# Optimization experiments

Measured on AMD Instinct MI355X. Metric: run time of the kernel, lower is better.

Reference implementation:

```python
import jax, jax.numpy as jnp
import numpy as np

EPS = 1e-3  # BatchNorm eps from partial(nn.BatchNorm1d, eps=0.001)


def _bn(x, g, b, m, v):
    # inference-mode BatchNorm1d with running stats
    return (x - m) * jax.lax.rsqrt(v + EPS) * g + b


def setup_inputs() -> dict:
    key = jax.random.key(0)
    ks = jax.random.split(key, 24)
    N_REF, N_Q, E = 50_000, 50_000, 1_600_000
    C_IN, C0, C1 = 16, 32, 32
    s = 0.1
    return {
        "ref_bxyz": jax.random.normal(ks[0], (N_REF, 4), jnp.float32),
        "ref_feat": jax.random.normal(ks[1], (N_REF, C_IN), jnp.float32),
        "query_bxyz": jax.random.normal(ks[2], (N_Q, 4), jnp.float32),
        "e_ref": jax.random.randint(ks[3], (E,), 0, N_REF, jnp.int32),
        "e_query": jax.random.randint(ks[4], (E,), 0, N_Q, jnp.int32),
        "w_pos": jax.random.normal(ks[5], (3, C0), jnp.float32) * s,
        "bn0_g": jax.random.uniform(ks[6], (C0,), jnp.float32, 0.5, 1.5),
        "bn0_b": jax.random.normal(ks[7], (C0,), jnp.float32) * s,
        "bn0_m": jax.random.normal(ks[8], (C0,), jnp.float32) * s,
        "bn0_v": jax.random.uniform(ks[9], (C0,), jnp.float32, 0.5, 1.5),
        "w_feat": jax.random.normal(ks[10], (C_IN, C0), jnp.float32) * s,
        "bnf_g": jax.random.uniform(ks[11], (C0,), jnp.float32, 0.5, 1.5),
        "bnf_b": jax.random.normal(ks[12], (C0,), jnp.float32) * s,
        "bnf_m": jax.random.normal(ks[13], (C0,), jnp.float32) * s,
        "bnf_v": jax.random.uniform(ks[14], (C0,), jnp.float32, 0.5, 1.5),
        "w1": jax.random.normal(ks[15], (C0, C1), jnp.float32) * s,
        "b1": jax.random.normal(ks[16], (C1,), jnp.float32) * s,
        "bn1_g": jax.random.uniform(ks[17], (C1,), jnp.float32, 0.5, 1.5),
        "bn1_b": jax.random.normal(ks[18], (C1,), jnp.float32) * s,
        "bn1_m": jax.random.normal(ks[19], (C1,), jnp.float32) * s,
        "bn1_v": jax.random.uniform(ks[20], (C1,), jnp.float32, 0.5, 1.5),
    }


def reference(ref_bxyz, ref_feat, query_bxyz, e_ref, e_query,
              w_pos, bn0_g, bn0_b, bn0_m, bn0_v,
              w_feat, bnf_g, bnf_b, bnf_m, bnf_v,
              w1, b1, bn1_g, bn1_b, bn1_m, bn1_v):
    # gather: per-edge xyz difference (drop batch column 0)
    pos_diff = (ref_bxyz[e_ref] - query_bxyz[e_query])[:, 1:4]        # [E, 3]
    pos_feat = _bn(pos_diff @ w_pos, bn0_g, bn0_b, bn0_m, bn0_v)       # [E, C0]
    # node-level feature projection, then gather per edge
    ref_feat2 = _bn(ref_feat @ w_feat, bnf_g, bnf_b, bnf_m, bnf_v)     # [N_ref, C0]
    edge_feat = jax.nn.relu(pos_feat + ref_feat2[e_ref])               # [E, C0]
    # mlp_convs chain (single layer here: C0 -> C1 with bias)
    edge_feat = jax.nn.relu(_bn(edge_feat @ w1 + b1, bn1_g, bn1_b, bn1_m, bn1_v))  # [E, C1]
    # scatter-max aggregate into query nodes; empty segments -> 0 (torch_scatter semantics)
    n_q = query_bxyz.shape[0]
    q = jax.ops.segment_max(edge_feat, e_query, num_segments=n_q)      # [N_q, C1]
    return jnp.where(jnp.isfinite(q), q, jnp.zeros((), q.dtype))
```

## Files before the change

### kernel.cpp

```cpp
#include <hip/hip_runtime.h>

#define EPS 1e-3f
#define FRAG_OFF 1184
#define PK_OFF 1696
#define NSUP 32
#define SUPSLOTS 69632
#define BINB 1024
#define WCAP 48
#define WRITERS 32
#define FCAP 1536
#define NFINE 2048

using frag_ab = __attribute__((ext_vector_type(8))) short;
using frag_cd = __attribute__((ext_vector_type(4))) float;
using iv4     = __attribute__((ext_vector_type(4))) int;

__device__ __forceinline__ unsigned pack_bf16_rne(float a, float b) {
    unsigned ua = __float_as_uint(a), ub = __float_as_uint(b);
    ua += 0x7FFFu + ((ua >> 16) & 1u);
    ub += 0x7FFFu + ((ub >> 16) & 1u);
    return (ua >> 16) | (ub & 0xFFFF0000u);
}
__device__ __forceinline__ unsigned cvt_pk_bf16(float a, float b) {
    unsigned r;
    asm("v_cvt_pk_bf16_f32 %0, %1, %2" : "=v"(r) : "v"(a), "v"(b));
    return r;
}
__device__ __forceinline__ float ubf_lo(unsigned u) { return __uint_as_float(u << 16); }
__device__ __forceinline__ float ubf_hi(unsigned u) { return __uint_as_float(u & 0xFFFF0000u); }

__global__ __launch_bounds__(256)
void mega_pre(const float* __restrict__ w_pos,
              const float* __restrict__ g0, const float* __restrict__ b0,
              const float* __restrict__ m0, const float* __restrict__ v0,
              const float* __restrict__ w1, const float* __restrict__ b1lin,
              const float* __restrict__ g1, const float* __restrict__ b1bn,
              const float* __restrict__ m1, const float* __restrict__ v1,
              const float* __restrict__ feat, const float* __restrict__ wf,
              const float* __restrict__ gf, const float* __restrict__ bf,
              const float* __restrict__ mf, const float* __restrict__ vf,
              const float4* __restrict__ bxyz,
              const int* __restrict__ e_query, const int* __restrict__ e_ref,
              float* __restrict__ ws, unsigned* __restrict__ ref2pk,
              uint2* __restrict__ pos_pk, int* __restrict__ supCur,
              unsigned* __restrict__ fineCnt, unsigned* __restrict__ pairs1,
              int E, int n_ref, int nodeB, int posB) {
    __shared__ unsigned bkt[4 * NSUP * WCAP];
    __shared__ int cnt[4 * NSUP];
    __shared__ int gb[NSUP], woff[4 * NSUP];

    int b = blockIdx.x, t = threadIdx.x;

    if (b == 0) {
        for (int i = t; i < NFINE; i += 256) fineCnt[i] = 0;
        if (t < 32) {
            int c = t;
            float s0 = g0[c] * rsqrtf(v0[c] + EPS);
            #pragma unroll
            for (int k = 0; k < 3; ++k) ws[k * 32 + c] = w_pos[k * 32 + c] * s0;
            ws[96 + c] = b0[c] - m0[c] * s0;
            float s1 = g1[c] * rsqrtf(v1[c] + EPS);
            #pragma unroll
            for (int k = 0; k < 32; ++k) ws[128 + k * 32 + c] = w1[k * 32 + c] * s1;
            ws[1152 + c] = (b1lin[c] - m1[c]) * s1 + b1bn[c];
        }
        __syncthreads();
        if (t < 64) {
            unsigned* wB = (unsigned*)ws + FRAG_OFF;
            int n = t & 15, quad = t >> 4;
            #pragma unroll
            for (int h = 0; h < 2; ++h) {
                int col = n + 16 * h;
                #pragma unroll
                for (int jp = 0; jp < 4; ++jp) {
                    int k = quad * 8 + 2 * jp;
                    wB[h * 256 + t * 4 + jp] =
                        pack_bf16_rne(ws[128 + k * 32 + col], ws[128 + (k + 1) * 32 + col]);
                }
            }
        }
        return;
    }
    b -= 1;
    if (b < nodeB) {
        int idx = b * 256 + t;
        if (idx < n_ref * 16) {
            int n = idx >> 4, cp = idx & 15;
            float fr[16];
            const float4* f4 = (const float4*)(feat + (size_t)n * 16);
            *(float4*)(fr)      = f4[0];
            *(float4*)(fr + 4)  = f4[1];
            *(float4*)(fr + 8)  = f4[2];
            *(float4*)(fr + 12) = f4[3];
            const float2* wf2 = (const float2*)wf;
            float a0 = 0.f, a1 = 0.f;
            #pragma unroll
            for (int k = 0; k < 16; ++k) {
                float2 wk = wf2[k * 16 + cp];
                a0 = fmaf(fr[k], wk.x, a0);
                a1 = fmaf(fr[k], wk.y, a1);
            }
            int c0 = 2 * cp, c1 = 2 * cp + 1;
            float s0 = gf[c0] * rsqrtf(vf[c0] + EPS);
            float s1 = gf[c1] * rsqrtf(vf[c1] + EPS);
            ref2pk[idx] = pack_bf16_rne((a0 - mf[c0]) * s0 + bf[c0],
                                        (a1 - mf[c1]) * s1 + bf[c1]);
        }
        return;
    }
    b -= nodeB;
    if (b < posB) {
        int i = b * 256 + t;
        if (i < n_ref) {
            float4 rb = bxyz[i];
            pos_pk[i] = make_uint2(pack_bf16_rne(rb.y, rb.z), pack_bf16_rne(rb.w, 0.f));
        }
        return;
    }
    b -= posB;
    int wv = t >> 6, lane = t & 63;
    if (t < 4 * NSUP) cnt[t] = 0;
    __syncthreads();
    int per = (((E + BINB * 4 - 1) / (BINB * 4)) + 3) & ~3;
    int gid = b * 4 + wv;
    int e0 = gid * per, e1 = min(e0 + per, E);
    for (int e = e0 + lane * 4; e < e1; e += 256) {
        if (e + 4 <= e1) {
            iv4 q4 = __builtin_nontemporal_load((const iv4*)(e_query + e));
            iv4 r4 = __builtin_nontemporal_load((const iv4*)(e_ref + e));
            #pragma unroll
            for (int j = 0; j < 4; ++j) {
                int q = q4[j], r = r4[j];
                int s = q >> 11;
                int pos = atomicAdd(&cnt[wv * NSUP + s], 1);
                if (pos < WCAP) bkt[wv * (NSUP * WCAP) + s * WCAP + pos] =
                    ((unsigned)(q & 2047) << 16) | (unsigned)r;
            }
        } else {
            for (int j = e; j < e1; ++j) {
                int q = e_query[j], r = e_ref[j];
                int s = q >> 11;
                int pos = atomicAdd(&cnt[wv * NSUP + s], 1);
                if (pos < WCAP) bkt[wv * (NSUP * WCAP) + s * WCAP + pos] =
                    ((unsigned)(q & 2047) << 16) | (unsigned)r;
            }
        }
    }
    __syncthreads();
    if (t < NSUP) {
        int s = t;
        int n0 = min(cnt[s], WCAP),            n1 = min(cnt[NSUP + s], WCAP);
        int n2 = min(cnt[2 * NSUP + s], WCAP), n3 = min(cnt[3 * NSUP + s], WCAP);
        woff[s] = 0; woff[NSUP + s] = n0;
        woff[2 * NSUP + s] = n0 + n1; woff[3 * NSUP + s] = n0 + n1 + n2;
        gb[s] = (n0 + n1 + n2 + n3) ? atomicAdd(&supCur[s], n0 + n1 + n2 + n3) : 0;
    }
    __syncthreads();
    for (int s = 0; s < NSUP; ++s) {
        int n = min(cnt[wv * NSUP + s], WCAP);
        if (lane < n) {
            int g = gb[s] + woff[wv * NSUP + s] + lane;
            if (g < SUPSLOTS)
                pairs1[(size_t)s * SUPSLOTS + g] = bkt[wv * (NSUP * WCAP) + s * WCAP + lane];
        }
    }
}

__global__ __launch_bounds__(256)
void finesort(const int* __restrict__ supCur, const unsigned* __restrict__ pairs1,
              unsigned* __restrict__ fineCnt, unsigned* __restrict__ pairs2) {
    __shared__ int h[64];
    __shared__ unsigned cb[64];
    __shared__ int lcnt[64];
    int s = blockIdx.x / WRITERS, w = blockIdx.x % WRITERS, t = threadIdx.x;
    if (t < 64) { h[t] = 0; lcnt[t] = 0; }
    __syncthreads();
    int n = min(supCur[s], SUPSLOTS);
    int lo = (n * w) / WRITERS, hi = (n * (w + 1)) / WRITERS;
    const unsigned* base = pairs1 + (size_t)s * SUPSLOTS;
    for (int i = lo + t; i < hi; i += 256)
        atomicAdd(&h[(base[i] >> 21) & 63], 1);
    __syncthreads();
    if (t < 64 && h[t] > 0)
        cb[t] = atomicAdd(&fineCnt[s * 64 + t], (unsigned)h[t]);
    __syncthreads();
    for (int i = lo + t; i < hi; i += 256) {
        unsigned u = base[i];
        int f = (u >> 21) & 63;
        unsigned pos = cb[f] + (unsigned)atomicAdd(&lcnt[f], 1);
        if (pos < FCAP)
            pairs2[(size_t)(s * 64 + f) * FCAP + pos] = u & 0x001FFFFFu;
    }
}

__global__ __launch_bounds__(512)
void fused_kernel(const uint2* __restrict__ pos_pk, const float4* __restrict__ query_bxyz,
                  const unsigned* __restrict__ fineCnt, const unsigned* __restrict__ pairs2,
                  const float* __restrict__ ws, float* __restrict__ out, int n_q) {
    __shared__ int outacc[32 * 33];
    __shared__ float4 qx[32];

    int t = threadIdx.x;
    int ln = t & 63, wv = t >> 6;
    int b = blockIdx.x;
    int q0 = b * 32;

    unsigned nc = fineCnt[b];
    int w = (int)(nc < FCAP ? nc : FCAP);
    const unsigned* __restrict__ src = pairs2 + (size_t)b * FCAP;
    if (t < 32) {
        int qq = q0 + t;
        qx[t] = query_bxyz[qq < n_q ? qq : 0];
    }
    for (int i = t; i < 32 * 33; i += 512) outacc[i] = 0;

    int mrow = ln & 15, cpg = ln >> 4;
    const float4* wsf4 = (const float4*)ws;
    float4 w0xa = wsf4[cpg * 2],          w0xb = wsf4[cpg * 2 + 1];
    float4 w0ya = wsf4[8 + cpg * 2],      w0yb = wsf4[8 + cpg * 2 + 1];
    float4 w0za = wsf4[16 + cpg * 2],     w0zb = wsf4[16 + cpg * 2 + 1];
    float4 b0a  = wsf4[24 + cpg * 2],     b0b  = wsf4[24 + cpg * 2 + 1];
    const int4* wB4 = (const int4*)((const unsigned*)ws + FRAG_OFF);
    frag_ab bfr0 = __builtin_bit_cast(frag_ab, wB4[ln]);
    frag_ab bfr1 = __builtin_bit_cast(frag_ab, wB4[64 + ln]);
    int ncol = ln & 15, quad = ln >> 4;
    float b1a = ws[1152 + ncol];
    float b1b = ws[1168 + ncol];
    const uint4* __restrict__ ref2pk = (const uint4*)((const unsigned*)ws + PK_OFF);
    __syncthreads();

    int nrt = (w + 15) >> 4;

    auto ldu = [&](int rt) -> unsigned {
        if (rt >= nrt) return 0u;
        int sg = rt * 16 + mrow;
        int idx = sg < w ? sg : (w - 1);
        return __builtin_nontemporal_load(src + idx);
    };

    unsigned u_c = 0;
    uint2 pp_c = {}; uint4 rf_c = {}; float4 qb_c = {};
    if (wv < nrt) {
        u_c = ldu(wv);
        int r = u_c & 0xFFFFu;
        pp_c = pos_pk[r];
        rf_c = ref2pk[r * 4 + cpg];
        qb_c = qx[u_c >> 16];
    }
    unsigned u_n = ldu(wv + 8);

    for (int rt = wv; rt < nrt; rt += 8) {
        int rtn = rt + 8;
        uint2 pp_n = {}; uint4 rf_n = {}; float4 qb_n = {};
        if (rtn < nrt) {
            int rn = u_n & 0xFFFFu;
            pp_n = pos_pk[rn];
            rf_n = ref2pk[rn * 4 + cpg];
            qb_n = qx[u_n >> 16];
        }
        unsigned u_n2 = ldu(rtn + 8);

        int lq = u_c >> 16;
        float d0 = ubf_lo(pp_c.x) - qb_c.y;
        float d1 = ubf_hi(pp_c.x) - qb_c.z;
        float d2 = ubf_lo(pp_c.y) - qb_c.w;
        float h0 = fmaxf(fmaf(d0, w0xa.x, fmaf(d1, w0ya.x, fmaf(d2, w0za.x, b0a.x))) + ubf_lo(rf_c.x), 0.f);
        float h1 = fmaxf(fmaf(d0, w0xa.y, fmaf(d1, w0ya.y, fmaf(d2, w0za.y, b0a.y))) + ubf_hi(rf_c.x), 0.f);
        float h2 = fmaxf(fmaf(d0, w0xa.z, fmaf(d1, w0ya.z, fmaf(d2, w0za.z, b0a.z))) + ubf_lo(rf_c.y), 0.f);
        float h3 = fmaxf(fmaf(d0, w0xa.w, fmaf(d1, w0ya.w, fmaf(d2, w0za.w, b0a.w))) + ubf_hi(rf_c.y), 0.f);
        float h4 = fmaxf(fmaf(d0, w0xb.x, fmaf(d1, w0yb.x, fmaf(d2, w0zb.x, b0b.x))) + ubf_lo(rf_c.z), 0.f);
        float h5 = fmaxf(fmaf(d0, w0xb.y, fmaf(d1, w0yb.y, fmaf(d2, w0zb.y, b0b.y))) + ubf_hi(rf_c.z), 0.f);
        float h6 = fmaxf(fmaf(d0, w0xb.z, fmaf(d1, w0yb.z, fmaf(d2, w0zb.z, b0b.z))) + ubf_lo(rf_c.w), 0.f);
        float h7 = fmaxf(fmaf(d0, w0xb.w, fmaf(d1, w0yb.w, fmaf(d2, w0zb.w, b0b.w))) + ubf_hi(rf_c.w), 0.f);
        int4 ai = make_int4((int)cvt_pk_bf16(h0, h1), (int)cvt_pk_bf16(h2, h3),
                            (int)cvt_pk_bf16(h4, h5), (int)cvt_pk_bf16(h6, h7));
        frag_ab af = __builtin_bit_cast(frag_ab, ai);
        frag_cd c0 = {b1a, b1a, b1a, b1a};
        frag_cd c1 = {b1b, b1b, b1b, b1b};
        c0 = __builtin_amdgcn_mfma_f32_16x16x32_bf16(af, bfr0, c0, 0, 0, 0);
        c1 = __builtin_amdgcn_mfma_f32_16x16x32_bf16(af, bfr1, c1, 0, 0, 0);
        int baserow = rt * 16 + quad * 4;
        #pragma unroll
        for (int rg = 0; rg < 4; ++rg) {
            int lqr = __shfl(lq, quad * 4 + rg, 64);
            if (baserow + rg < w) {
                atomicMax(&outacc[ncol * 33 + lqr], __float_as_int(c0[rg]));
                atomicMax(&outacc[(ncol + 16) * 33 + lqr], __float_as_int(c1[rg]));
            }
        }
        u_c = u_n; pp_c = pp_n; rf_c = rf_n; qb_c = qb_n;
        u_n = u_n2;
    }
    __syncthreads();
    #pragma unroll
    for (int g = 0; g < 2; ++g) {
        int o = t + 512 * g;
        int qq = o >> 5, ch = o & 31;
        int qo = q0 + qq;
        if (qo < n_q)
            __builtin_nontemporal_store(__int_as_float(outacc[ch * 33 + qq]),
                                        out + (size_t)qo * 32 + ch);
    }
}

extern "C" void kernel_launch(void* const* d_in, const int* in_sizes, int n_in,
                              void* d_out, int out_size, void* d_ws, size_t ws_size,
                              hipStream_t stream) {
    const float* ref_bxyz   = (const float*)d_in[0];
    const float* ref_feat   = (const float*)d_in[1];
    const float* query_bxyz = (const float*)d_in[2];
    const int*   e_ref      = (const int*)d_in[3];
    const int*   e_query    = (const int*)d_in[4];
    const float* w_pos      = (const float*)d_in[5];
    const float* bn0_g = (const float*)d_in[6];
    const float* bn0_b = (const float*)d_in[7];
    const float* bn0_m = (const float*)d_in[8];
    const float* bn0_v = (const float*)d_in[9];
    const float* w_feat = (const float*)d_in[10];
    const float* bnf_g = (const float*)d_in[11];
    const float* bnf_b = (const float*)d_in[12];
    const float* bnf_m = (const float*)d_in[13];
    const float* bnf_v = (const float*)d_in[14];
    const float* w1    = (const float*)d_in[15];
    const float* b1    = (const float*)d_in[16];
    const float* bn1_g = (const float*)d_in[17];
    const float* bn1_b = (const float*)d_in[18];
    const float* bn1_m = (const float*)d_in[19];
    const float* bn1_v = (const float*)d_in[20];

    int n_ref = in_sizes[0] / 4;
    int n_q   = in_sizes[2] / 4;
    int E     = in_sizes[3];
    int nb    = (n_q + 31) >> 5;

    float* ws = (float*)d_ws;
    unsigned* base_u = (unsigned*)d_ws;
    size_t off = PK_OFF;
    unsigned* ref2pk = base_u + off;           off += (size_t)n_ref * 16;
    uint2*    pos_pk = (uint2*)(base_u + off); off += (size_t)n_ref * 2;
    int*      supCur = (int*)(base_u + off);   off += NSUP;
    unsigned* fineCnt = base_u + off;          off += NFINE;
    off = (off + 63) & ~(size_t)63;
    unsigned* pairs1 = base_u + off;           off += (size_t)NSUP * SUPSLOTS;
    unsigned* pairs2 = base_u + off;           off += (size_t)nb * FCAP;

    int nodeB = (n_ref * 16 + 255) / 256;
    int posB  = (n_ref + 255) / 256;

    hipMemsetAsync(supCur, 0, NSUP * sizeof(int), stream);

    int megaGrid = 1 + nodeB + posB + BINB;
    mega_pre<<<megaGrid, 256, 0, stream>>>(
        w_pos, bn0_g, bn0_b, bn0_m, bn0_v, w1, b1, bn1_g, bn1_b, bn1_m, bn1_v,
        ref_feat, w_feat, bnf_g, bnf_b, bnf_m, bnf_v,
        (const float4*)ref_bxyz, e_query, e_ref,
        ws, ref2pk, pos_pk, supCur, fineCnt, pairs1, E, n_ref, nodeB, posB);

    finesort<<<NSUP * WRITERS, 256, 0, stream>>>(supCur, pairs1, fineCnt, pairs2);

    fused_kernel<<<nb, 512, 0, stream>>>(
        pos_pk, (const float4*)query_bxyz,
        fineCnt, pairs2, ws, (float*)d_out, n_q);
}
```

Before: 172.8 us.

## Restructure coarse binning with block-wide buckets, grid-stride prefetch, padded counters

```diff
diff --git a/kernel.cpp b/kernel.cpp
--- a/kernel.cpp
+++ b/kernel.cpp
@@ -6,7 +6,7 @@
 #define NSUP 32
 #define SUPSLOTS 69632
 #define BINB 1024
-#define WCAP 48
+#define WCAPB 128
 #define WRITERS 32
 #define FCAP 1536
 #define NFINE 2048
@@ -45,9 +45,9 @@
               uint2* __restrict__ pos_pk, int* __restrict__ supCur,
               unsigned* __restrict__ fineCnt, unsigned* __restrict__ pairs1,
               int E, int n_ref, int nodeB, int posB) {
-    __shared__ unsigned bkt[4 * NSUP * WCAP];
-    __shared__ int cnt[4 * NSUP];
-    __shared__ int gb[NSUP], woff[4 * NSUP];
+    __shared__ unsigned bkt[NSUP * WCAPB];
+    __shared__ int cnt[NSUP];
+    __shared__ int gb[NSUP];
 
     int b = blockIdx.x, t = threadIdx.x;
 
@@ -118,50 +118,58 @@
         return;
     }
     b -= posB;
-    int wv = t >> 6, lane = t & 63;
-    if (t < 4 * NSUP) cnt[t] = 0;
-    __syncthreads();
-    int per = (((E + BINB * 4 - 1) / (BINB * 4)) + 3) & ~3;
-    int gid = b * 4 + wv;
-    int e0 = gid * per, e1 = min(e0 + per, E);
-    for (int e = e0 + lane * 4; e < e1; e += 256) {
-        if (e + 4 <= e1) {
-            iv4 q4 = __builtin_nontemporal_load((const iv4*)(e_query + e));
-            iv4 r4 = __builtin_nontemporal_load((const iv4*)(e_ref + e));
-            #pragma unroll
-            for (int j = 0; j < 4; ++j) {
-                int q = q4[j], r = r4[j];
+    for (int i = t; i < NSUP; i += 256) cnt[i] = 0;
+    __syncthreads();
+    const int STRIDE = BINB * 256 * 4;
+    int idx = (b * 256 + t) * 4;
+
+    iv4 qc = {}, rc = {};
+    bool vc = idx < E;
+    bool fc = vc && (idx + 4 <= E);
+    if (fc) {
+        qc = __builtin_nontemporal_load((const iv4*)(e_query + idx));
+        rc = __builtin_nontemporal_load((const iv4*)(e_ref + idx));
+    } else if (vc) {
+        for (int j = 0; j < 4; ++j)
+            if (idx + j < E) { qc[j] = e_query[idx + j]; rc[j] = e_ref[idx + j]; }
+    }
+    while (vc) {
+        int idx2 = idx + STRIDE;
+        bool vn = idx2 < E;
+        bool fn = vn && (idx2 + 4 <= E);
+        iv4 qn = {}, rn = {};
+        if (fn) {
+            qn = __builtin_nontemporal_load((const iv4*)(e_query + idx2));
+            rn = __builtin_nontemporal_load((const iv4*)(e_ref + idx2));
+        } else if (vn) {
+            for (int j = 0; j < 4; ++j)
+                if (idx2 + j < E) { qn[j] = e_query[idx2 + j]; rn[j] = e_ref[idx2 + j]; }
+        }
+        int lim = E - idx;
+        #pragma unroll
+        for (int j = 0; j < 4; ++j) {
+            if (j < lim) {
+                int q = qc[j], r = rc[j];
                 int s = q >> 11;
-                int pos = atomicAdd(&cnt[wv * NSUP + s], 1);
-                if (pos < WCAP) bkt[wv * (NSUP * WCAP) + s * WCAP + pos] =
+                int pos = atomicAdd(&cnt[s], 1);
+                if (pos < WCAPB) bkt[s * WCAPB + pos] =
                     ((unsigned)(q & 2047) << 16) | (unsigned)r;
             }
-        } else {
-            for (int j = e; j < e1; ++j) {
-                int q = e_query[j], r = e_ref[j];
-                int s = q >> 11;
-                int pos = atomicAdd(&cnt[wv * NSUP + s], 1);
-                if (pos < WCAP) bkt[wv * (NSUP * WCAP) + s * WCAP + pos] =
-                    ((unsigned)(q & 2047) << 16) | (unsigned)r;
-            }
-        }
+        }
+        qc = qn; rc = rn; vc = vn; idx = idx2;
     }
     __syncthreads();
     if (t < NSUP) {
-        int s = t;
-        int n0 = min(cnt[s], WCAP),            n1 = min(cnt[NSUP + s], WCAP);
-        int n2 = min(cnt[2 * NSUP + s], WCAP), n3 = min(cnt[3 * NSUP + s], WCAP);
-        woff[s] = 0; woff[NSUP + s] = n0;
-        woff[2 * NSUP + s] = n0 + n1; woff[3 * NSUP + s] = n0 + n1 + n2;
-        gb[s] = (n0 + n1 + n2 + n3) ? atomicAdd(&supCur[s], n0 + n1 + n2 + n3) : 0;
+        int n = min(cnt[t], WCAPB);
+        gb[t] = n ? atomicAdd(&supCur[t * 16], n) : 0;
     }
     __syncthreads();
     for (int s = 0; s < NSUP; ++s) {
-        int n = min(cnt[wv * NSUP + s], WCAP);
-        if (lane < n) {
-            int g = gb[s] + woff[wv * NSUP + s] + lane;
+        int n = min(cnt[s], WCAPB);
+        if (t < n) {
+            int g = gb[s] + t;
             if (g < SUPSLOTS)
-                pairs1[(size_t)s * SUPSLOTS + g] = bkt[wv * (NSUP * WCAP) + s * WCAP + lane];
+                pairs1[(size_t)s * SUPSLOTS + g] = bkt[s * WCAPB + t];
         }
     }
 }
@@ -175,21 +183,39 @@
     int s = blockIdx.x / WRITERS, w = blockIdx.x % WRITERS, t = threadIdx.x;
     if (t < 64) { h[t] = 0; lcnt[t] = 0; }
     __syncthreads();
-    int n = min(supCur[s], SUPSLOTS);
+    int n = min(supCur[s * 16], SUPSLOTS);
     int lo = (n * w) / WRITERS, hi = (n * (w + 1)) / WRITERS;
     const unsigned* base = pairs1 + (size_t)s * SUPSLOTS;
-    for (int i = lo + t; i < hi; i += 256)
-        atomicAdd(&h[(base[i] >> 21) & 63], 1);
+    {
+        int i = lo + t;
+        bool vc = i < hi;
+        unsigned cur = vc ? base[i] : 0u;
+        while (vc) {
+            int i2 = i + 256;
+            bool vn = i2 < hi;
+            unsigned nxt = vn ? base[i2] : 0u;
+            atomicAdd(&h[(cur >> 21) & 63], 1);
+            cur = nxt; vc = vn; i = i2;
+        }
+    }
     __syncthreads();
     if (t < 64 && h[t] > 0)
         cb[t] = atomicAdd(&fineCnt[s * 64 + t], (unsigned)h[t]);
     __syncthreads();
-    for (int i = lo + t; i < hi; i += 256) {
-        unsigned u = base[i];
-        int f = (u >> 21) & 63;
-        unsigned pos = cb[f] + (unsigned)atomicAdd(&lcnt[f], 1);
-        if (pos < FCAP)
-            pairs2[(size_t)(s * 64 + f) * FCAP + pos] = u & 0x001FFFFFu;
+    {
+        int i = lo + t;
+        bool vc = i < hi;
+        unsigned cur = vc ? base[i] : 0u;
+        while (vc) {
+            int i2 = i + 256;
+            bool vn = i2 < hi;
+            unsigned nxt = vn ? base[i2] : 0u;
+            int f = (cur >> 21) & 63;
+            unsigned pos = cb[f] + (unsigned)atomicAdd(&lcnt[f], 1);
+            if (pos < FCAP)
+                pairs2[(size_t)(s * 64 + f) * FCAP + pos] = cur & 0x001FFFFFu;
+            cur = nxt; vc = vn; i = i2;
+        }
     }
 }
 
@@ -338,7 +364,7 @@
     size_t off = PK_OFF;
     unsigned* ref2pk = base_u + off;           off += (size_t)n_ref * 16;
     uint2*    pos_pk = (uint2*)(base_u + off); off += (size_t)n_ref * 2;
-    int*      supCur = (int*)(base_u + off);   off += NSUP;
+    int*      supCur = (int*)(base_u + off);   off += NSUP * 16;
     unsigned* fineCnt = base_u + off;          off += NFINE;
     off = (off + 63) & ~(size_t)63;
     unsigned* pairs1 = base_u + off;           off += (size_t)NSUP * SUPSLOTS;
@@ -347,7 +373,7 @@
     int nodeB = (n_ref * 16 + 255) / 256;
     int posB  = (n_ref + 255) / 256;
 
-    hipMemsetAsync(supCur, 0, NSUP * sizeof(int), stream);
+    hipMemsetAsync(supCur, 0, NSUP * 16 * sizeof(int), stream);
 
     int megaGrid = 1 + nodeB + posB + BINB;
     mega_pre<<<megaGrid, 256, 0, stream>>>(
```

After: 175.9 us. About the same (+1.8%).

## Bin edges with one wave per 256 edges and pad supercell counters apart

Applied to the files above, without the earlier changes.

```diff
diff --git a/kernel.cpp b/kernel.cpp
--- a/kernel.cpp
+++ b/kernel.cpp
@@ -5,8 +5,7 @@
 #define PK_OFF 1696
 #define NSUP 32
 #define SUPSLOTS 69632
-#define BINB 1024
-#define WCAP 48
+#define WCAP 40
 #define WRITERS 32
 #define FCAP 1536
 #define NFINE 2048
@@ -121,28 +120,28 @@
     int wv = t >> 6, lane = t & 63;
     if (t < 4 * NSUP) cnt[t] = 0;
     __syncthreads();
-    int per = (((E + BINB * 4 - 1) / (BINB * 4)) + 3) & ~3;
-    int gid = b * 4 + wv;
-    int e0 = gid * per, e1 = min(e0 + per, E);
-    for (int e = e0 + lane * 4; e < e1; e += 256) {
-        if (e + 4 <= e1) {
-            iv4 q4 = __builtin_nontemporal_load((const iv4*)(e_query + e));
-            iv4 r4 = __builtin_nontemporal_load((const iv4*)(e_ref + e));
+    {
+        int gidw = b * 4 + wv;
+        int e0 = gidw * 256;
+        int e1 = min(e0 + 256, E);
+        int e = e0 + lane * 4;
+        if (e < e1) {
+            iv4 q4 = {}, r4 = {};
+            if (e + 4 <= e1) {
+                q4 = __builtin_nontemporal_load((const iv4*)(e_query + e));
+                r4 = __builtin_nontemporal_load((const iv4*)(e_ref + e));
+            } else {
+                for (int j = 0; e + j < e1; ++j) { q4[j] = e_query[e + j]; r4[j] = e_ref[e + j]; }
+            }
             #pragma unroll
             for (int j = 0; j < 4; ++j) {
-                int q = q4[j], r = r4[j];
-                int s = q >> 11;
-                int pos = atomicAdd(&cnt[wv * NSUP + s], 1);
-                if (pos < WCAP) bkt[wv * (NSUP * WCAP) + s * WCAP + pos] =
-                    ((unsigned)(q & 2047) << 16) | (unsigned)r;
-            }
-        } else {
-            for (int j = e; j < e1; ++j) {
-                int q = e_query[j], r = e_ref[j];
-                int s = q >> 11;
-                int pos = atomicAdd(&cnt[wv * NSUP + s], 1);
-                if (pos < WCAP) bkt[wv * (NSUP * WCAP) + s * WCAP + pos] =
-                    ((unsigned)(q & 2047) << 16) | (unsigned)r;
+                if (e + j < e1) {
+                    int q = q4[j], r = r4[j];
+                    int s = q >> 11;
+                    int pos = atomicAdd(&cnt[wv * NSUP + s], 1);
+                    if (pos < WCAP) bkt[wv * (NSUP * WCAP) + s * WCAP + pos] =
+                        ((unsigned)(q & 2047) << 16) | (unsigned)r;
+                }
             }
         }
     }
@@ -153,7 +152,8 @@
         int n2 = min(cnt[2 * NSUP + s], WCAP), n3 = min(cnt[3 * NSUP + s], WCAP);
         woff[s] = 0; woff[NSUP + s] = n0;
         woff[2 * NSUP + s] = n0 + n1; woff[3 * NSUP + s] = n0 + n1 + n2;
-        gb[s] = (n0 + n1 + n2 + n3) ? atomicAdd(&supCur[s], n0 + n1 + n2 + n3) : 0;
+        int tot = n0 + n1 + n2 + n3;
+        gb[s] = tot ? atomicAdd(&supCur[s * 16], tot) : 0;
     }
     __syncthreads();
     for (int s = 0; s < NSUP; ++s) {
@@ -175,7 +175,7 @@
     int s = blockIdx.x / WRITERS, w = blockIdx.x % WRITERS, t = threadIdx.x;
     if (t < 64) { h[t] = 0; lcnt[t] = 0; }
     __syncthreads();
-    int n = min(supCur[s], SUPSLOTS);
+    int n = min(supCur[s * 16], SUPSLOTS);
     int lo = (n * w) / WRITERS, hi = (n * (w + 1)) / WRITERS;
     const unsigned* base = pairs1 + (size_t)s * SUPSLOTS;
     for (int i = lo + t; i < hi; i += 256)
@@ -338,7 +338,7 @@
     size_t off = PK_OFF;
     unsigned* ref2pk = base_u + off;           off += (size_t)n_ref * 16;
     uint2*    pos_pk = (uint2*)(base_u + off); off += (size_t)n_ref * 2;
-    int*      supCur = (int*)(base_u + off);   off += NSUP;
+    int*      supCur = (int*)(base_u + off);   off += NSUP * 16;
     unsigned* fineCnt = base_u + off;          off += NFINE;
     off = (off + 63) & ~(size_t)63;
     unsigned* pairs1 = base_u + off;           off += (size_t)NSUP * SUPSLOTS;
@@ -346,10 +346,11 @@
 
     int nodeB = (n_ref * 16 + 255) / 256;
     int posB  = (n_ref + 255) / 256;
-
-    hipMemsetAsync(supCur, 0, NSUP * sizeof(int), stream);
-
-    int megaGrid = 1 + nodeB + posB + BINB;
+    int binB  = (E + 1023) / 1024;
+
+    hipMemsetAsync(supCur, 0, NSUP * 16 * sizeof(int), stream);
+
+    int megaGrid = 1 + nodeB + posB + binB;
     mega_pre<<<megaGrid, 256, 0, stream>>>(
         w_pos, bn0_g, bn0_b, bn0_m, bn0_v, w1, b1, bn1_g, bn1_b, bn1_m, bn1_v,
         ref_feat, w_feat, bnf_g, bnf_b, bnf_m, bnf_v,
```

New measurement: 188.0 us. +8.8%, slower.
